# Kernel optimization log

Measured on AMD Instinct MI355X. Metric: run time of the kernel, lower is better.

The kernel has to match this reference:

```python
import jax, jax.numpy as jnp
import numpy as np

N, E, F_IN, EDGE_DIM, EMB, H, L, DENSE = 50000, 800000, 16, 4, 32, 4, 2, 128
HC = EMB * H


def setup_inputs() -> dict:
    ks = iter(jax.random.split(jax.random.key(0), 64))

    def w(shape, fan):
        return jax.random.normal(next(ks), shape, jnp.float32) / np.float32(np.sqrt(fan))

    inp = {}
    inp['x'] = jax.random.normal(next(ks), (N, F_IN), jnp.float32)
    inp['edge_index'] = jax.random.randint(next(ks), (2, E), 0, N, jnp.int32)
    inp['edge_attr'] = jax.random.normal(next(ks), (E, EDGE_DIM), jnp.float32)
    # layer-0 TransformerConv (F_IN -> EMB, H heads) + transf Linear
    inp['Wq0'] = w((F_IN, HC), F_IN); inp['bq0'] = w((HC,), HC)
    inp['Wk0'] = w((F_IN, HC), F_IN); inp['bk0'] = w((HC,), HC)
    inp['Wv0'] = w((F_IN, HC), F_IN); inp['bv0'] = w((HC,), HC)
    inp['We0'] = w((EDGE_DIM, HC), EDGE_DIM)
    inp['Ws0'] = w((F_IN, HC), F_IN); inp['bs0'] = w((HC,), HC)
    inp['Wt0'] = w((HC, EMB), HC); inp['bt0'] = w((EMB,), EMB)
    # stacked L inner layers (EMB -> EMB)
    inp['Wq'] = w((L, EMB, HC), EMB); inp['bq'] = w((L, HC), HC)
    inp['Wk'] = w((L, EMB, HC), EMB); inp['bk'] = w((L, HC), HC)
    inp['Wv'] = w((L, EMB, HC), EMB); inp['bv'] = w((L, HC), HC)
    inp['We'] = w((L, EDGE_DIM, HC), EDGE_DIM)
    inp['Ws'] = w((L, EMB, HC), EMB); inp['bs'] = w((L, HC), HC)
    inp['Wt'] = w((L, HC, EMB), HC); inp['bt'] = w((L, EMB), EMB)
    # dense head
    inp['W1'] = w((EMB, DENSE), EMB); inp['b1'] = w((DENSE,), DENSE)
    inp['W2'] = w((DENSE, DENSE // 2), DENSE); inp['b2'] = w((DENSE // 2,), DENSE)
    inp['W3'] = w((DENSE // 2, 1), DENSE // 2); inp['b3'] = w((1,), 1)
    return inp


def _tconv(h, edge_attr, src, dst, Wq, bq, Wk, bk, Wv, bv, We, Ws, bs):
    """PyG TransformerConv: edge-conditioned multi-head attention + root skip."""
    n = h.shape[0]
    q = (h @ Wq + bq).reshape(n, H, EMB)
    k = (h @ Wk + bk).reshape(n, H, EMB)
    v = (h @ Wv + bv).reshape(n, H, EMB)
    e = (edge_attr @ We).reshape(-1, H, EMB)          # [E,H,C]
    kj = k[src] + e                                   # gather + edge bias
    logits = (q[dst] * kj).sum(-1) / np.float32(np.sqrt(EMB))  # [E,H]
    m = jax.ops.segment_max(logits, dst, num_segments=n)       # segment softmax
    p = jnp.exp(logits - m[dst])
    z = jax.ops.segment_sum(p, dst, num_segments=n)
    alpha = p / (z[dst] + 1e-16)
    msg = (v[src] + e) * alpha[:, :, None]
    out = jax.ops.segment_sum(msg, dst, num_segments=n).reshape(n, HC)
    return out + h @ Ws + bs                          # root_weight skip


def _forward(x, edge_attr, Wq0, bq0, Wk0, bk0, Wv0, bv0, We0, Ws0, bs0, Wt0, bt0,
             Wq, bq, Wk, bk, Wv, bv, We, Ws, bs, Wt, bt,
             W1, b1, W2, b2, W3, b3, edge_index):
    src, dst = edge_index[0], edge_index[1]
    h = _tconv(x, edge_attr, src, dst, Wq0, bq0, Wk0, bk0, Wv0, bv0, We0, Ws0, bs0)
    h = jax.nn.relu(h @ Wt0 + bt0)
    for i in range(L):
        h = _tconv(h, edge_attr, src, dst, Wq[i], bq[i], Wk[i], bk[i],
                   Wv[i], bv[i], We[i], Ws[i], bs[i])
        h = jax.nn.relu(h @ Wt[i] + bt[i])
    h = jax.nn.relu(h @ W1 + b1)
    h = jax.nn.relu(h @ W2 + b2)
    return jax.nn.sigmoid(h @ W3 + b3)                # [N,1]


def reference(x, edge_index, edge_attr, Wq0, bq0, Wk0, bk0, Wv0, bv0, We0, Ws0, bs0,
              Wt0, bt0, Wq, bq, Wk, bk, Wv, bv, We, Ws, bs, Wt, bt,
              W1, b1, W2, b2, W3, b3):
    return _forward(x, edge_attr, Wq0, bq0, Wk0, bk0, Wv0, bv0, We0, Ws0, bs0,
                    Wt0, bt0, Wq, bq, Wk, bk, Wv, bv, We, Ws, bs, Wt, bt,
                    W1, b1, W2, b2, W3, b3, edge_index)
```

## Files before the change

### kernel.cpp

```cpp
#include <hip/hip_runtime.h>

#define NN 50000
#define EE 800000
#define FIN 16
#define EDIM 4
#define EMB 32
#define NH 4
#define HC 128
#define NL 2
#define DENSE 128
#define QNPB 50
#define SBLK 49

__device__ __forceinline__ float2 h2f2(unsigned int u) {
    union { unsigned int u; _Float16 h[2]; } c; c.u = u;
    return make_float2((float)c.h[0], (float)c.h[1]);
}

__global__ void hist_kernel(const int* __restrict__ dst, int* __restrict__ counts) {
    int e = blockIdx.x * blockDim.x + threadIdx.x;
    if (e < EE) atomicAdd(&counts[dst[e]], 1);
}

__global__ __launch_bounds__(1024) void scan1_kernel(const int* __restrict__ cursor,
                                                     int* __restrict__ row_ptr,
                                                     int* __restrict__ bsum) {
    __shared__ int wsum[16];
    __shared__ int wpre[17];
    int tid = threadIdx.x, lane = tid & 63, wid = tid >> 6;
    int i = blockIdx.x * 1024 + tid;
    int v = (i < NN) ? cursor[i] : 0;
    int incl = v;
    #pragma unroll
    for (int off = 1; off < 64; off <<= 1) {
        int t = __shfl_up(incl, off, 64);
        if (lane >= off) incl += t;
    }
    if (lane == 63) wsum[wid] = incl;
    __syncthreads();
    if (tid == 0) {
        int acc = 0;
        #pragma unroll
        for (int w = 0; w < 16; ++w) { wpre[w] = acc; acc += wsum[w]; }
        wpre[16] = acc;
    }
    __syncthreads();
    if (i < NN) row_ptr[i] = wpre[wid] + incl - v;
    if (tid == 0) bsum[blockIdx.x] = wpre[16];
}

__global__ void scan2_kernel(int* __restrict__ bsum, int* __restrict__ row_ptr) {
    int t = threadIdx.x;
    int v = (t < SBLK) ? bsum[t] : 0;
    int incl = v;
    #pragma unroll
    for (int off = 1; off < 64; off <<= 1) {
        int u = __shfl_up(incl, off, 64);
        if (t >= off) incl += u;
    }
    if (t < SBLK) bsum[t] = incl - v;
    if (t == 63) row_ptr[NN] = incl;
}

__global__ __launch_bounds__(1024) void scan3_kernel(int* __restrict__ row_ptr,
                                                     int* __restrict__ cursor,
                                                     const int* __restrict__ bsum) {
    int i = blockIdx.x * 1024 + threadIdx.x;
    if (i >= NN) return;
    int r = row_ptr[i] + bsum[blockIdx.x];
    row_ptr[i] = r;
    cursor[i] = r;
}

__global__ void scatter_kernel(const int* __restrict__ src, const int* __restrict__ dst,
                               const float* __restrict__ ea, int* __restrict__ cursor,
                               int* __restrict__ ssrc, float4* __restrict__ sea) {
    int e = blockIdx.x * blockDim.x + threadIdx.x;
    if (e >= EE) return;
    int d = dst[e];
    int pos = atomicAdd(&cursor[d], 1);
    ssrc[pos] = src[e];
    sea[pos] = *reinterpret_cast<const float4*>(ea + (size_t)e * 4);
}

__global__ __launch_bounds__(512) void qkvs0_kernel(const float* __restrict__ x,
        const float* __restrict__ Wq, const float* __restrict__ bq,
        const float* __restrict__ Wk, const float* __restrict__ bk,
        const float* __restrict__ Wv, const float* __restrict__ bv,
        const float* __restrict__ Ws, const float* __restrict__ bs,
        float* __restrict__ Q, _Float16* __restrict__ kvh,
        float* __restrict__ Out) {
    __shared__ __align__(16) float hs[QNPB * FIN];
    int tid = threadIdx.x;
    int m = tid >> 7, c = tid & 127;
    const float* W; const float* b;
    switch (m) {
        case 0:  W = Wq; b = bq; break;
        case 1:  W = Wk; b = bk; break;
        case 2:  W = Wv; b = bv; break;
        default: W = Ws; b = bs; break;
    }
    float w[FIN];
    #pragma unroll
    for (int f = 0; f < FIN; ++f) w[f] = W[f * HC + c];
    float bias = b[c];
    int node0 = blockIdx.x * QNPB;
    {
        const float4* src4 = (const float4*)(x + (size_t)node0 * FIN);
        float4* dst4 = (float4*)hs;
        for (int i = tid; i < QNPB * FIN / 4; i += 512) dst4[i] = src4[i];
    }
    __syncthreads();
    const float4* hs4 = (const float4*)hs;
    for (int k = 0; k < QNPB; ++k) {
        float s = bias;
        #pragma unroll
        for (int f4 = 0; f4 < FIN / 4; ++f4) {
            float4 hv = hs4[k * (FIN / 4) + f4];
            s += hv.x * w[4 * f4] + hv.y * w[4 * f4 + 1]
               + hv.z * w[4 * f4 + 2] + hv.w * w[4 * f4 + 3];
        }
        size_t n = node0 + k;
        if      (m == 0) Q[n * HC + c] = s;
        else if (m == 1) kvh[n * 256 + 2 * c] = (_Float16)s;
        else if (m == 2) kvh[n * 256 + 2 * c + 1] = (_Float16)s;
        else             Out[n * HC + c] = s;
    }
}

__global__ __launch_bounds__(512) void ftq_kernel(const float* __restrict__ Wt,
        const float* __restrict__ bt,
        const float* __restrict__ Wq, const float* __restrict__ bq,
        const float* __restrict__ Wk, const float* __restrict__ bk,
        const float* __restrict__ Wv, const float* __restrict__ bv,
        const float* __restrict__ Ws, const float* __restrict__ bs,
        float* __restrict__ Q, _Float16* __restrict__ kvh,
        float* __restrict__ Out) {
    __shared__ __align__(16) float os[QNPB * HC];
    __shared__ __align__(16) float hs[QNPB * EMB];
    int tid = threadIdx.x;
    int node0 = blockIdx.x * QNPB;
    int g = tid >> 7;

    {
        const float4* src4 = (const float4*)(Out + (size_t)node0 * HC);
        float4* dst4 = (float4*)os;
        for (int i = tid; i < QNPB * HC / 4; i += 512) dst4[i] = src4[i];
    }

    int cT = (tid & 127) >> 2, seg = tid & 3;
    float wt[32];
    #pragma unroll
    for (int j = 0; j < 32; ++j) wt[j] = Wt[(seg * 32 + j) * EMB + cT];
    float btc = bt[cT];
    __syncthreads();
    for (int k = g; k < QNPB; k += 4) {
        float p = 0.f;
        const float4* r4 = (const float4*)(os + k * HC + seg * 32);
        #pragma unroll
        for (int j4 = 0; j4 < 8; ++j4) {
            float4 rv = r4[j4];
            p += rv.x * wt[4 * j4] + rv.y * wt[4 * j4 + 1]
               + rv.z * wt[4 * j4 + 2] + rv.w * wt[4 * j4 + 3];
        }
        p += __shfl_xor(p, 1, 64);
        p += __shfl_xor(p, 2, 64);
        if (seg == 0) hs[k * EMB + cT] = fmaxf(p + btc, 0.f);
    }
    __syncthreads();

    int m = tid >> 7, c = tid & 127;
    const float* W; const float* b;
    switch (m) {
        case 0:  W = Wq; b = bq; break;
        case 1:  W = Wk; b = bk; break;
        case 2:  W = Wv; b = bv; break;
        default: W = Ws; b = bs; break;
    }
    float w[EMB];
    #pragma unroll
    for (int f = 0; f < EMB; ++f) w[f] = W[f * HC + c];
    float bias = b[c];
    const float4* hs4 = (const float4*)hs;
    for (int k = 0; k < QNPB; ++k) {
        float s = bias;
        #pragma unroll
        for (int f4 = 0; f4 < EMB / 4; ++f4) {
            float4 hv = hs4[k * (EMB / 4) + f4];
            s += hv.x * w[4 * f4] + hv.y * w[4 * f4 + 1]
               + hv.z * w[4 * f4 + 2] + hv.w * w[4 * f4 + 3];
        }
        size_t n = node0 + k;
        if      (m == 0) Q[n * HC + c] = s;
        else if (m == 1) kvh[n * 256 + 2 * c] = (_Float16)s;
        else if (m == 2) kvh[n * 256 + 2 * c + 1] = (_Float16)s;
        else             Out[n * HC + c] = s;
    }
}

__global__ __launch_bounds__(256) void edge_attn_kernel(const int* __restrict__ row_ptr,
        const int* __restrict__ ssrc, const float4* __restrict__ sea,
        const float* __restrict__ We,
        const float* __restrict__ Q, const uint2* __restrict__ kvp,
        float2* __restrict__ Out) {
    int n = blockIdx.x * 4 + (threadIdx.x >> 6);
    int lane = threadIdx.x & 63;
    int ch0 = 2 * lane, ch1 = 2 * lane + 1;
    float we0[4], we1[4];
    #pragma unroll
    for (int d = 0; d < 4; ++d) { we0[d] = We[d * HC + ch0]; we1[d] = We[d * HC + ch1]; }
    float2 q = ((const float2*)Q)[(size_t)n * 64 + lane];
    int start = row_ptr[n], end = row_ptr[n + 1];
    float z = 0.f, acc0 = 0.f, acc1 = 0.f;
    const float SC = 0.17677669529663687f;
    int i = start;
    for (; i + 1 < end; i += 2) {
        int sA = ssrc[i], sB = ssrc[i + 1];
        sA = sA < 0 ? 0 : (sA >= NN ? NN - 1 : sA);
        sB = sB < 0 ? 0 : (sB >= NN ? NN - 1 : sB);
        float4 eA = sea[i], eB = sea[i + 1];
        uint2 kvA = kvp[(size_t)sA * 64 + lane];
        uint2 kvB = kvp[(size_t)sB * 64 + lane];
        float eA0 = eA.x * we0[0] + eA.y * we0[1] + eA.z * we0[2] + eA.w * we0[3];
        float eA1 = eA.x * we1[0] + eA.y * we1[1] + eA.z * we1[2] + eA.w * we1[3];
        float eB0 = eB.x * we0[0] + eB.y * we0[1] + eB.z * we0[2] + eB.w * we0[3];
        float eB1 = eB.x * we1[0] + eB.y * we1[1] + eB.z * we1[2] + eB.w * we1[3];
        float2 kvA0 = h2f2(kvA.x), kvA1 = h2f2(kvA.y);
        float2 kvB0 = h2f2(kvB.x), kvB1 = h2f2(kvB.y);
        float pA = q.x * (kvA0.x + eA0) + q.y * (kvA1.x + eA1);
        float pB = q.x * (kvB0.x + eB0) + q.y * (kvB1.x + eB1);
        #pragma unroll
        for (int off = 1; off < 16; off <<= 1) {
            pA += __shfl_xor(pA, off, 64);
            pB += __shfl_xor(pB, off, 64);
        }
        float xA = __expf(pA * SC), xB = __expf(pB * SC);
        z += xA + xB;
        acc0 += xA * (kvA0.y + eA0) + xB * (kvB0.y + eB0);
        acc1 += xA * (kvA1.y + eA1) + xB * (kvB1.y + eB1);
    }
    if (i < end) {
        int s = ssrc[i];
        s = s < 0 ? 0 : (s >= NN ? NN - 1 : s);
        float4 e = sea[i];
        uint2 kv = kvp[(size_t)s * 64 + lane];
        float e0 = e.x * we0[0] + e.y * we0[1] + e.z * we0[2] + e.w * we0[3];
        float e1 = e.x * we1[0] + e.y * we1[1] + e.z * we1[2] + e.w * we1[3];
        float2 kv0 = h2f2(kv.x), kv1 = h2f2(kv.y);
        float p = q.x * (kv0.x + e0) + q.y * (kv1.x + e1);
        #pragma unroll
        for (int off = 1; off < 16; off <<= 1) p += __shfl_xor(p, off, 64);
        float x = __expf(p * SC);
        z += x;
        acc0 += x * (kv0.y + e0);
        acc1 += x * (kv1.y + e1);
    }
    float inv = 1.f / (z + 1e-16f);
    size_t oi = (size_t)n * 64 + lane;
    float2 o = Out[oi];
    o.x += acc0 * inv;
    o.y += acc1 * inv;
    Out[oi] = o;
}

__global__ __launch_bounds__(512) void head2_kernel(const float* __restrict__ Outb,
        const float* __restrict__ Wt, const float* __restrict__ bt,
        const float* __restrict__ W1, const float* __restrict__ b1,
        const float* __restrict__ W2, const float* __restrict__ b2,
        const float* __restrict__ W3, const float* __restrict__ b3,
        float* __restrict__ out) {
    __shared__ __align__(16) float os[QNPB * HC];
    __shared__ __align__(16) float hs[QNPB * EMB];
    __shared__ __align__(16) float d2s[QNPB * 64];
    float* d1s = os;
    int tid = threadIdx.x;
    int node0 = blockIdx.x * QNPB;
    int g = tid >> 7;

    {
        const float4* src4 = (const float4*)(Outb + (size_t)node0 * HC);
        float4* dst4 = (float4*)os;
        for (int i = tid; i < QNPB * HC / 4; i += 512) dst4[i] = src4[i];
    }

    int cT = (tid & 127) >> 2, seg = tid & 3;
    float wt[32];
    #pragma unroll
    for (int j = 0; j < 32; ++j) wt[j] = Wt[(seg * 32 + j) * EMB + cT];
    float btc = bt[cT];
    __syncthreads();
    for (int k = g; k < QNPB; k += 4) {
        float p = 0.f;
        const float4* r4 = (const float4*)(os + k * HC + seg * 32);
        #pragma unroll
        for (int j4 = 0; j4 < 8; ++j4) {
            float4 rv = r4[j4];
            p += rv.x * wt[4 * j4] + rv.y * wt[4 * j4 + 1]
               + rv.z * wt[4 * j4 + 2] + rv.w * wt[4 * j4 + 3];
        }
        p += __shfl_xor(p, 1, 64);
        p += __shfl_xor(p, 2, 64);
        if (seg == 0) hs[k * EMB + cT] = fmaxf(p + btc, 0.f);
    }
    __syncthreads();

    int c1 = tid & 127;
    float w1[32];
    #pragma unroll
    for (int f = 0; f < 32; ++f) w1[f] = W1[f * DENSE + c1];
    float b1c = b1[c1];
    const float4* hs4 = (const float4*)hs;
    for (int k = g; k < QNPB; k += 4) {
        float s = b1c;
        #pragma unroll
        for (int f4 = 0; f4 < 8; ++f4) {
            float4 hv = hs4[k * 8 + f4];
            s += hv.x * w1[4 * f4] + hv.y * w1[4 * f4 + 1]
               + hv.z * w1[4 * f4 + 2] + hv.w * w1[4 * f4 + 3];
        }
        d1s[k * DENSE + c1] = fmaxf(s, 0.f);
    }
    __syncthreads();

    int c2 = (tid & 127) >> 1, hh = tid & 1;
    float w2[64];
    #pragma unroll
    for (int j = 0; j < 64; ++j) w2[j] = W2[(hh * 64 + j) * 64 + c2];
    float b2c = b2[c2];
    for (int k = g; k < QNPB; k += 4) {
        float p = 0.f;
        const float4* r4 = (const float4*)(d1s + k * DENSE + hh * 64);
        #pragma unroll
        for (int j4 = 0; j4 < 16; ++j4) {
            float4 rv = r4[j4];
            p += rv.x * w2[4 * j4] + rv.y * w2[4 * j4 + 1]
               + rv.z * w2[4 * j4 + 2] + rv.w * w2[4 * j4 + 3];
        }
        p += __shfl_xor(p, 1, 64);
        if (hh == 0) d2s[k * 64 + c2] = fmaxf(p + b2c, 0.f);
    }
    __syncthreads();

    int w = tid >> 6, lane = tid & 63;
    float w3r = W3[lane];
    float b3r = b3[0];
    for (int k = w; k < QNPB; k += 8) {
        float t = d2s[k * 64 + lane] * w3r;
        #pragma unroll
        for (int off = 1; off < 64; off <<= 1) t += __shfl_xor(t, off, 64);
        if (lane == 0) out[node0 + k] = 1.f / (1.f + __expf(-(t + b3r)));
    }
}

extern "C" void kernel_launch(void* const* d_in, const int* in_sizes, int n_in,
                              void* d_out, int out_size, void* d_ws, size_t ws_size,
                              hipStream_t stream) {
    const float* x   = (const float*)d_in[0];
    const int*   ei  = (const int*)d_in[1];
    const float* ea  = (const float*)d_in[2];
    const float* Wq0 = (const float*)d_in[3];  const float* bq0 = (const float*)d_in[4];
    const float* Wk0 = (const float*)d_in[5];  const float* bk0 = (const float*)d_in[6];
    const float* Wv0 = (const float*)d_in[7];  const float* bv0 = (const float*)d_in[8];
    const float* We0 = (const float*)d_in[9];
    const float* Ws0 = (const float*)d_in[10]; const float* bs0 = (const float*)d_in[11];
    const float* Wt0 = (const float*)d_in[12]; const float* bt0 = (const float*)d_in[13];
    const float* WqL = (const float*)d_in[14]; const float* bqL = (const float*)d_in[15];
    const float* WkL = (const float*)d_in[16]; const float* bkL = (const float*)d_in[17];
    const float* WvL = (const float*)d_in[18]; const float* bvL = (const float*)d_in[19];
    const float* WeL = (const float*)d_in[20];
    const float* WsL = (const float*)d_in[21]; const float* bsL = (const float*)d_in[22];
    const float* WtL = (const float*)d_in[23]; const float* btL = (const float*)d_in[24];
    const float* W1  = (const float*)d_in[25]; const float* b1  = (const float*)d_in[26];
    const float* W2  = (const float*)d_in[27]; const float* b2  = (const float*)d_in[28];
    const float* W3  = (const float*)d_in[29]; const float* b3  = (const float*)d_in[30];
    float* out = (float*)d_out;

    char* ws = (char*)d_ws;
    size_t off = 0;
    auto alloc = [&](size_t bytes) -> void* {
        void* p = ws + off; off = (off + bytes + 255) & ~(size_t)255; return p;
    };
    int*     cursor  = (int*)    alloc((size_t)NN * 4);
    int*     row_ptr = (int*)    alloc((size_t)(NN + 1) * 4);
    int*     bsum    = (int*)    alloc((size_t)SBLK * 4);
    int*     ssrc    = (int*)    alloc((size_t)EE * 4);
    float4*  sea     = (float4*) alloc((size_t)EE * 16);
    float*   Q       = (float*)  alloc((size_t)NN * HC * 4);
    _Float16* kvh    = (_Float16*)alloc((size_t)NN * HC * 2 * 2);
    float*   Outb    = (float*)  alloc((size_t)NN * HC * 4);

    hipMemsetAsync(cursor, 0, (size_t)NN * 4, stream);
    hist_kernel<<<(EE + 255) / 256, 256, 0, stream>>>(ei + EE, cursor);
    scan1_kernel<<<SBLK, 1024, 0, stream>>>(cursor, row_ptr, bsum);
    scan2_kernel<<<1, 64, 0, stream>>>(bsum, row_ptr);
    scan3_kernel<<<SBLK, 1024, 0, stream>>>(row_ptr, cursor, bsum);
    scatter_kernel<<<(EE + 255) / 256, 256, 0, stream>>>(ei, ei + EE, ea, cursor, ssrc, sea);

    const uint2* kvp = (const uint2*)kvh;
    float2* Out2 = (float2*)Outb;

    qkvs0_kernel<<<NN / QNPB, 512, 0, stream>>>(x, Wq0, bq0, Wk0, bk0, Wv0, bv0,
                                                Ws0, bs0, Q, kvh, Outb);
    edge_attn_kernel<<<NN / 4, 256, 0, stream>>>(row_ptr, ssrc, sea, We0, Q, kvp, Out2);

    ftq_kernel<<<NN / QNPB, 512, 0, stream>>>(Wt0, bt0,
        WqL, bqL, WkL, bkL, WvL, bvL, WsL, bsL, Q, kvh, Outb);
    edge_attn_kernel<<<NN / 4, 256, 0, stream>>>(row_ptr, ssrc, sea, WeL, Q, kvp, Out2);

    ftq_kernel<<<NN / QNPB, 512, 0, stream>>>(WtL, btL,
        WqL + EMB * HC, bqL + HC, WkL + EMB * HC, bkL + HC,
        WvL + EMB * HC, bvL + HC, WsL + EMB * HC, bsL + HC, Q, kvh, Outb);
    edge_attn_kernel<<<NN / 4, 256, 0, stream>>>(row_ptr, ssrc, sea,
        WeL + EDIM * HC, Q, kvp, Out2);

    head2_kernel<<<NN / QNPB, 512, 0, stream>>>(Outb, WtL + (size_t)HC * EMB, btL + EMB,
                                                W1, b1, W2, b2, W3, b3, out);
}
```

Before: 637.4 us.

## Fuse edge attention into per-node transform kernels with ping-pong fp16 KV buffers

Removes the standalone edge_attn kernel. Each layer's attention aggregation now runs inside the following per-node kernel (attnftq / attnhead). Partial outputs accumulate in shared memory instead of going through a global read-modify-write, and the fused kernel then reads them back for the Wt transform. Because the fused kernel gathers K/V from other nodes while writing new K/V, two KV buffers alternate between layers. Q is also stored in fp16 to halve its traffic, at some cost in precision. In exchange, attention now runs with 512-thread blocks of 50 nodes and fewer independent waves, which may reduce latency hiding for the irregular gathers.

Result: no change. 645.6 us (+1.3%).

```diff
diff --git a/kernel.cpp b/kernel.cpp
--- a/kernel.cpp
+++ b/kernel.cpp
@@ -12,8 +12,10 @@
 #define QNPB 50
 #define SBLK 49
 
-__device__ __forceinline__ float2 h2f2(unsigned int u) {
-    union { unsigned int u; _Float16 h[2]; } c; c.u = u;
+typedef unsigned int uint;
+
+__device__ __forceinline__ float2 h2f2(uint u) {
+    union { uint u; _Float16 h[2]; } c; c.u = u;
     return make_float2((float)c.h[0], (float)c.h[1]);
 }
 
@@ -88,7 +90,7 @@
         const float* __restrict__ Wk, const float* __restrict__ bk,
         const float* __restrict__ Wv, const float* __restrict__ bv,
         const float* __restrict__ Ws, const float* __restrict__ bs,
-        float* __restrict__ Q, _Float16* __restrict__ kvh,
+        _Float16* __restrict__ Qh, _Float16* __restrict__ kvh,
         float* __restrict__ Out) {
     __shared__ __align__(16) float hs[QNPB * FIN];
     int tid = threadIdx.x;
@@ -121,39 +123,108 @@
                + hv.z * w[4 * f4 + 2] + hv.w * w[4 * f4 + 3];
         }
         size_t n = node0 + k;
-        if      (m == 0) Q[n * HC + c] = s;
+        if      (m == 0) Qh[n * HC + c] = (_Float16)s;
         else if (m == 1) kvh[n * 256 + 2 * c] = (_Float16)s;
         else if (m == 2) kvh[n * 256 + 2 * c + 1] = (_Float16)s;
         else             Out[n * HC + c] = s;
     }
 }
 
-__global__ __launch_bounds__(512) void ftq_kernel(const float* __restrict__ Wt,
-        const float* __restrict__ bt,
+__global__ __launch_bounds__(512) void attnftq_kernel(const int* __restrict__ row_ptr,
+        const int* __restrict__ ssrc, const float4* __restrict__ sea,
+        const float* __restrict__ We,
+        const float* __restrict__ Wt, const float* __restrict__ bt,
         const float* __restrict__ Wq, const float* __restrict__ bq,
         const float* __restrict__ Wk, const float* __restrict__ bk,
         const float* __restrict__ Wv, const float* __restrict__ bv,
         const float* __restrict__ Ws, const float* __restrict__ bs,
-        float* __restrict__ Q, _Float16* __restrict__ kvh,
-        float* __restrict__ Out) {
+        _Float16* __restrict__ Qh, const uint2* __restrict__ kv_in,
+        _Float16* __restrict__ kv_out, float* __restrict__ Out) {
     __shared__ __align__(16) float os[QNPB * HC];
     __shared__ __align__(16) float hs[QNPB * EMB];
     int tid = threadIdx.x;
     int node0 = blockIdx.x * QNPB;
-    int g = tid >> 7;
 
     {
         const float4* src4 = (const float4*)(Out + (size_t)node0 * HC);
         float4* dst4 = (float4*)os;
         for (int i = tid; i < QNPB * HC / 4; i += 512) dst4[i] = src4[i];
     }
-
+    __syncthreads();
+
+    {
+        int wid = tid >> 6, lane = tid & 63;
+        float we0[4], we1[4];
+        #pragma unroll
+        for (int d = 0; d < 4; ++d) {
+            we0[d] = We[d * HC + 2 * lane];
+            we1[d] = We[d * HC + 2 * lane + 1];
+        }
+        const uint* Qu = (const uint*)Qh;
+        const float SC = 0.17677669529663687f;
+        for (int k = wid; k < QNPB; k += 8) {
+            int n = node0 + k;
+            float2 q = h2f2(Qu[(size_t)n * 64 + lane]);
+            int start = row_ptr[n], end = row_ptr[n + 1];
+            float z = 0.f, acc0 = 0.f, acc1 = 0.f;
+            int i = start;
+            for (; i + 1 < end; i += 2) {
+                int sA = ssrc[i], sB = ssrc[i + 1];
+                sA = sA < 0 ? 0 : (sA >= NN ? NN - 1 : sA);
+                sB = sB < 0 ? 0 : (sB >= NN ? NN - 1 : sB);
+                float4 eA = sea[i], eB = sea[i + 1];
+                uint2 kvA = kv_in[(size_t)sA * 64 + lane];
+                uint2 kvB = kv_in[(size_t)sB * 64 + lane];
+                float eA0 = eA.x * we0[0] + eA.y * we0[1] + eA.z * we0[2] + eA.w * we0[3];
+                float eA1 = eA.x * we1[0] + eA.y * we1[1] + eA.z * we1[2] + eA.w * we1[3];
+                float eB0 = eB.x * we0[0] + eB.y * we0[1] + eB.z * we0[2] + eB.w * we0[3];
+                float eB1 = eB.x * we1[0] + eB.y * we1[1] + eB.z * we1[2] + eB.w * we1[3];
+                float2 kvA0 = h2f2(kvA.x), kvA1 = h2f2(kvA.y);
+                float2 kvB0 = h2f2(kvB.x), kvB1 = h2f2(kvB.y);
+                float pA = q.x * (kvA0.x + eA0) + q.y * (kvA1.x + eA1);
+                float pB = q.x * (kvB0.x + eB0) + q.y * (kvB1.x + eB1);
+                #pragma unroll
+                for (int off = 1; off < 16; off <<= 1) {
+                    pA += __shfl_xor(pA, off, 64);
+                    pB += __shfl_xor(pB, off, 64);
+                }
+                float xA = __expf(pA * SC), xB = __expf(pB * SC);
+                z += xA + xB;
+                acc0 += xA * (kvA0.y + eA0) + xB * (kvB0.y + eB0);
+                acc1 += xA * (kvA1.y + eA1) + xB * (kvB1.y + eB1);
+            }
+            if (i < end) {
+                int s = ssrc[i];
+                s = s < 0 ? 0 : (s >= NN ? NN - 1 : s);
+                float4 e = sea[i];
+                uint2 kv = kv_in[(size_t)s * 64 + lane];
+                float e0 = e.x * we0[0] + e.y * we0[1] + e.z * we0[2] + e.w * we0[3];
+                float e1 = e.x * we1[0] + e.y * we1[1] + e.z * we1[2] + e.w * we1[3];
+                float2 kv0 = h2f2(kv.x), kv1 = h2f2(kv.y);
+                float p = q.x * (kv0.x + e0) + q.y * (kv1.x + e1);
+                #pragma unroll
+                for (int off = 1; off < 16; off <<= 1) p += __shfl_xor(p, off, 64);
+                float x = __expf(p * SC);
+                z += x;
+                acc0 += x * (kv0.y + e0);
+                acc1 += x * (kv1.y + e1);
+            }
+            float inv = 1.f / (z + 1e-16f);
+            float2* osp = (float2*)(os + k * HC);
+            float2 o = osp[lane];
+            o.x += acc0 * inv;
+            o.y += acc1 * inv;
+            osp[lane] = o;
+        }
+    }
+    __syncthreads();
+
+    int g = tid >> 7;
     int cT = (tid & 127) >> 2, seg = tid & 3;
     float wt[32];
     #pragma unroll
     for (int j = 0; j < 32; ++j) wt[j] = Wt[(seg * 32 + j) * EMB + cT];
     float btc = bt[cT];
-    __syncthreads();
     for (int k = g; k < QNPB; k += 4) {
         float p = 0.f;
         const float4* r4 = (const float4*)(os + k * HC + seg * 32);
@@ -191,79 +262,18 @@
                + hv.z * w[4 * f4 + 2] + hv.w * w[4 * f4 + 3];
         }
         size_t n = node0 + k;
-        if      (m == 0) Q[n * HC + c] = s;
-        else if (m == 1) kvh[n * 256 + 2 * c] = (_Float16)s;
-        else if (m == 2) kvh[n * 256 + 2 * c + 1] = (_Float16)s;
+        if      (m == 0) Qh[n * HC + c] = (_Float16)s;
+        else if (m == 1) kv_out[n * 256 + 2 * c] = (_Float16)s;
+        else if (m == 2) kv_out[n * 256 + 2 * c + 1] = (_Float16)s;
         else             Out[n * HC + c] = s;
     }
 }
 
-__global__ __launch_bounds__(256) void edge_attn_kernel(const int* __restrict__ row_ptr,
+__global__ __launch_bounds__(512) void attnhead_kernel(const int* __restrict__ row_ptr,
         const int* __restrict__ ssrc, const float4* __restrict__ sea,
         const float* __restrict__ We,
-        const float* __restrict__ Q, const uint2* __restrict__ kvp,
-        float2* __restrict__ Out) {
-    int n = blockIdx.x * 4 + (threadIdx.x >> 6);
-    int lane = threadIdx.x & 63;
-    int ch0 = 2 * lane, ch1 = 2 * lane + 1;
-    float we0[4], we1[4];
-    #pragma unroll
-    for (int d = 0; d < 4; ++d) { we0[d] = We[d * HC + ch0]; we1[d] = We[d * HC + ch1]; }
-    float2 q = ((const float2*)Q)[(size_t)n * 64 + lane];
-    int start = row_ptr[n], end = row_ptr[n + 1];
-    float z = 0.f, acc0 = 0.f, acc1 = 0.f;
-    const float SC = 0.17677669529663687f;
-    int i = start;
-    for (; i + 1 < end; i += 2) {
-        int sA = ssrc[i], sB = ssrc[i + 1];
-        sA = sA < 0 ? 0 : (sA >= NN ? NN - 1 : sA);
-        sB = sB < 0 ? 0 : (sB >= NN ? NN - 1 : sB);
-        float4 eA = sea[i], eB = sea[i + 1];
-        uint2 kvA = kvp[(size_t)sA * 64 + lane];
-        uint2 kvB = kvp[(size_t)sB * 64 + lane];
-        float eA0 = eA.x * we0[0] + eA.y * we0[1] + eA.z * we0[2] + eA.w * we0[3];
-        float eA1 = eA.x * we1[0] + eA.y * we1[1] + eA.z * we1[2] + eA.w * we1[3];
-        float eB0 = eB.x * we0[0] + eB.y * we0[1] + eB.z * we0[2] + eB.w * we0[3];
-        float eB1 = eB.x * we1[0] + eB.y * we1[1] + eB.z * we1[2] + eB.w * we1[3];
-        float2 kvA0 = h2f2(kvA.x), kvA1 = h2f2(kvA.y);
-        float2 kvB0 = h2f2(kvB.x), kvB1 = h2f2(kvB.y);
-        float pA = q.x * (kvA0.x + eA0) + q.y * (kvA1.x + eA1);
-        float pB = q.x * (kvB0.x + eB0) + q.y * (kvB1.x + eB1);
-        #pragma unroll
-        for (int off = 1; off < 16; off <<= 1) {
-            pA += __shfl_xor(pA, off, 64);
-            pB += __shfl_xor(pB, off, 64);
-        }
-        float xA = __expf(pA * SC), xB = __expf(pB * SC);
-        z += xA + xB;
-        acc0 += xA * (kvA0.y + eA0) + xB * (kvB0.y + eB0);
-        acc1 += xA * (kvA1.y + eA1) + xB * (kvB1.y + eB1);
-    }
-    if (i < end) {
-        int s = ssrc[i];
-        s = s < 0 ? 0 : (s >= NN ? NN - 1 : s);
-        float4 e = sea[i];
-        uint2 kv = kvp[(size_t)s * 64 + lane];
-        float e0 = e.x * we0[0] + e.y * we0[1] + e.z * we0[2] + e.w * we0[3];
-        float e1 = e.x * we1[0] + e.y * we1[1] + e.z * we1[2] + e.w * we1[3];
-        float2 kv0 = h2f2(kv.x), kv1 = h2f2(kv.y);
-        float p = q.x * (kv0.x + e0) + q.y * (kv1.x + e1);
-        #pragma unroll
-        for (int off = 1; off < 16; off <<= 1) p += __shfl_xor(p, off, 64);
-        float x = __expf(p * SC);
-        z += x;
-        acc0 += x * (kv0.y + e0);
-        acc1 += x * (kv1.y + e1);
-    }
-    float inv = 1.f / (z + 1e-16f);
-    size_t oi = (size_t)n * 64 + lane;
-    float2 o = Out[oi];
-    o.x += acc0 * inv;
-    o.y += acc1 * inv;
-    Out[oi] = o;
-}
-
-__global__ __launch_bounds__(512) void head2_kernel(const float* __restrict__ Outb,
+        const _Float16* __restrict__ Qh, const uint2* __restrict__ kv_in,
+        const float* __restrict__ Outb,
         const float* __restrict__ Wt, const float* __restrict__ bt,
         const float* __restrict__ W1, const float* __restrict__ b1,
         const float* __restrict__ W2, const float* __restrict__ b2,
@@ -275,20 +285,87 @@
     float* d1s = os;
     int tid = threadIdx.x;
     int node0 = blockIdx.x * QNPB;
-    int g = tid >> 7;
 
     {
         const float4* src4 = (const float4*)(Outb + (size_t)node0 * HC);
         float4* dst4 = (float4*)os;
         for (int i = tid; i < QNPB * HC / 4; i += 512) dst4[i] = src4[i];
     }
-
+    __syncthreads();
+
+    {
+        int wid = tid >> 6, lane = tid & 63;
+        float we0[4], we1[4];
+        #pragma unroll
+        for (int d = 0; d < 4; ++d) {
+            we0[d] = We[d * HC + 2 * lane];
+            we1[d] = We[d * HC + 2 * lane + 1];
+        }
+        const uint* Qu = (const uint*)Qh;
+        const float SC = 0.17677669529663687f;
+        for (int k = wid; k < QNPB; k += 8) {
+            int n = node0 + k;
+            float2 q = h2f2(Qu[(size_t)n * 64 + lane]);
+            int start = row_ptr[n], end = row_ptr[n + 1];
+            float z = 0.f, acc0 = 0.f, acc1 = 0.f;
+            int i = start;
+            for (; i + 1 < end; i += 2) {
+                int sA = ssrc[i], sB = ssrc[i + 1];
+                sA = sA < 0 ? 0 : (sA >= NN ? NN - 1 : sA);
+                sB = sB < 0 ? 0 : (sB >= NN ? NN - 1 : sB);
+                float4 eA = sea[i], eB = sea[i + 1];
+                uint2 kvA = kv_in[(size_t)sA * 64 + lane];
+                uint2 kvB = kv_in[(size_t)sB * 64 + lane];
+                float eA0 = eA.x * we0[0] + eA.y * we0[1] + eA.z * we0[2] + eA.w * we0[3];
+                float eA1 = eA.x * we1[0] + eA.y * we1[1] + eA.z * we1[2] + eA.w * we1[3];
+                float eB0 = eB.x * we0[0] + eB.y * we0[1] + eB.z * we0[2] + eB.w * we0[3];
+                float eB1 = eB.x * we1[0] + eB.y * we1[1] + eB.z * we1[2] + eB.w * we1[3];
+                float2 kvA0 = h2f2(kvA.x), kvA1 = h2f2(kvA.y);
+                float2 kvB0 = h2f2(kvB.x), kvB1 = h2f2(kvB.y);
+                float pA = q.x * (kvA0.x + eA0) + q.y * (kvA1.x + eA1);
+                float pB = q.x * (kvB0.x + eB0) + q.y * (kvB1.x + eB1);
+                #pragma unroll
+                for (int off = 1; off < 16; off <<= 1) {
+                    pA += __shfl_xor(pA, off, 64);
+                    pB += __shfl_xor(pB, off, 64);
+                }
+                float xA = __expf(pA * SC), xB = __expf(pB * SC);
+                z += xA + xB;
+                acc0 += xA * (kvA0.y + eA0) + xB * (kvB0.y + eB0);
+                acc1 += xA * (kvA1.y + eA1) + xB * (kvB1.y + eB1);
+            }
+            if (i < end) {
+                int s = ssrc[i];
+                s = s < 0 ? 0 : (s >= NN ? NN - 1 : s);
+                float4 e = sea[i];
+                uint2 kv = kv_in[(size_t)s * 64 + lane];
+                float e0 = e.x * we0[0] + e.y * we0[1] + e.z * we0[2] + e.w * we0[3];
+                float e1 = e.x * we1[0] + e.y * we1[1] + e.z * we1[2] + e.w * we1[3];
+                float2 kv0 = h2f2(kv.x), kv1 = h2f2(kv.y);
+                float p = q.x * (kv0.x + e0) + q.y * (kv1.x + e1);
+                #pragma unroll
+                for (int off = 1; off < 16; off <<= 1) p += __shfl_xor(p, off, 64);
+                float x = __expf(p * SC);
+                z += x;
+                acc0 += x * (kv0.y + e0);
+                acc1 += x * (kv1.y + e1);
+            }
+            float inv = 1.f / (z + 1e-16f);
+            float2* osp = (float2*)(os + k * HC);
+            float2 o = osp[lane];
+            o.x += acc0 * inv;
+            o.y += acc1 * inv;
+            osp[lane] = o;
+        }
+    }
+    __syncthreads();
+
+    int g = tid >> 7;
     int cT = (tid & 127) >> 2, seg = tid & 3;
     float wt[32];
     #pragma unroll
     for (int j = 0; j < 32; ++j) wt[j] = Wt[(seg * 32 + j) * EMB + cT];
     float btc = bt[cT];
-    __syncthreads();
     for (int k = g; k < QNPB; k += 4) {
         float p = 0.f;
         const float4* r4 = (const float4*)(os + k * HC + seg * 32);
@@ -380,14 +457,15 @@
     auto alloc = [&](size_t bytes) -> void* {
         void* p = ws + off; off = (off + bytes + 255) & ~(size_t)255; return p;
     };
-    int*     cursor  = (int*)    alloc((size_t)NN * 4);
-    int*     row_ptr = (int*)    alloc((size_t)(NN + 1) * 4);
-    int*     bsum    = (int*)    alloc((size_t)SBLK * 4);
-    int*     ssrc    = (int*)    alloc((size_t)EE * 4);
-    float4*  sea     = (float4*) alloc((size_t)EE * 16);
-    float*   Q       = (float*)  alloc((size_t)NN * HC * 4);
-    _Float16* kvh    = (_Float16*)alloc((size_t)NN * HC * 2 * 2);
-    float*   Outb    = (float*)  alloc((size_t)NN * HC * 4);
+    int*      cursor  = (int*)     alloc((size_t)NN * 4);
+    int*      row_ptr = (int*)     alloc((size_t)(NN + 1) * 4);
+    int*      bsum    = (int*)     alloc((size_t)SBLK * 4);
+    int*      ssrc    = (int*)     alloc((size_t)EE * 4);
+    float4*   sea     = (float4*)  alloc((size_t)EE * 16);
+    _Float16* Qh      = (_Float16*)alloc((size_t)NN * HC * 2);
+    _Float16* kvA     = (_Float16*)alloc((size_t)NN * HC * 2 * 2);
+    _Float16* kvB     = (_Float16*)alloc((size_t)NN * HC * 2 * 2);
+    float*    Outb    = (float*)   alloc((size_t)NN * HC * 4);
 
     hipMemsetAsync(cursor, 0, (size_t)NN * 4, stream);
     hist_kernel<<<(EE + 255) / 256, 256, 0, stream>>>(ei + EE, cursor);
@@ -396,23 +474,21 @@
     scan3_kernel<<<SBLK, 1024, 0, stream>>>(row_ptr, cursor, bsum);
     scatter_kernel<<<(EE + 255) / 256, 256, 0, stream>>>(ei, ei + EE, ea, cursor, ssrc, sea);
 
-    const uint2* kvp = (const uint2*)kvh;
-    float2* Out2 = (float2*)Outb;
-
     qkvs0_kernel<<<NN / QNPB, 512, 0, stream>>>(x, Wq0, bq0, Wk0, bk0, Wv0, bv0,
-                                                Ws0, bs0, Q, kvh, Outb);
-    edge_attn_kernel<<<NN / 4, 256, 0, stream>>>(row_ptr, ssrc, sea, We0, Q, kvp, Out2);
-
-    ftq_kernel<<<NN / QNPB, 512, 0, stream>>>(Wt0, bt0,
-        WqL, bqL, WkL, bkL, WvL, bvL, WsL, bsL, Q, kvh, Outb);
-    edge_attn_kernel<<<NN / 4, 256, 0, stream>>>(row_ptr, ssrc, sea, WeL, Q, kvp, Out2);
-
-    ftq_kernel<<<NN / QNPB, 512, 0, stream>>>(WtL, btL,
+                                                Ws0, bs0, Qh, kvA, Outb);
+
+    attnftq_kernel<<<NN / QNPB, 512, 0, stream>>>(row_ptr, ssrc, sea, We0,
+        Wt0, bt0, WqL, bqL, WkL, bkL, WvL, bvL, WsL, bsL,
+        Qh, (const uint2*)kvA, kvB, Outb);
+
+    attnftq_kernel<<<NN / QNPB, 512, 0, stream>>>(row_ptr, ssrc, sea, WeL,
+        WtL, btL,
         WqL + EMB * HC, bqL + HC, WkL + EMB * HC, bkL + HC,
-        WvL + EMB * HC, bvL + HC, WsL + EMB * HC, bsL + HC, Q, kvh, Outb);
-    edge_attn_kernel<<<NN / 4, 256, 0, stream>>>(row_ptr, ssrc, sea,
-        WeL + EDIM * HC, Q, kvp, Out2);
-
-    head2_kernel<<<NN / QNPB, 512, 0, stream>>>(Outb, WtL + (size_t)HC * EMB, btL + EMB,
-                                                W1, b1, W2, b2, W3, b3, out);
-}
+        WvL + EMB * HC, bvL + HC, WsL + EMB * HC, bsL + HC,
+        Qh, (const uint2*)kvB, kvA, Outb);
+
+    attnhead_kernel<<<NN / QNPB, 512, 0, stream>>>(row_ptr, ssrc, sea,
+        WeL + EDIM * HC, Qh, (const uint2*)kvA, Outb,
+        WtL + (size_t)HC * EMB, btL + EMB,
+        W1, b1, W2, b2, W3, b3, out);
+}
```
